# Optimization experiments

Hardware: AMD Instinct MI355X
Metric: run time of the kernel (lower is better)

## Reference

```python
import jax, jax.numpy as jnp
import numpy as np

D_EMBED = 768
D_HEAD = 64
B, S = 4, 4096


def setup_inputs() -> dict:
    key = jax.random.key(0)
    ks = jax.random.split(key, 8)
    x = jax.random.normal(ks[0], (B, S, D_EMBED), dtype=jnp.float32)
    mask = jax.random.randint(ks[1], (B, S), 0, 2, dtype=jnp.int32)
    s = 1.0 / np.sqrt(D_EMBED)
    Wq = jax.random.normal(ks[2], (D_EMBED, D_HEAD), dtype=jnp.float32) * s
    bq = jnp.zeros((D_HEAD,), dtype=jnp.float32)
    Wk = jax.random.normal(ks[3], (D_EMBED, D_HEAD), dtype=jnp.float32) * s
    bk = jnp.zeros((D_HEAD,), dtype=jnp.float32)
    Wv = jax.random.normal(ks[4], (D_EMBED, D_HEAD), dtype=jnp.float32) * s
    bv = jnp.zeros((D_HEAD,), dtype=jnp.float32)
    return {"x": x, "mask": mask, "Wq": Wq, "bq": bq, "Wk": Wk, "bk": bk, "Wv": Wv, "bv": bv}


def reference(x, mask, Wq, bq, Wk, bk, Wv, bv):
    # x: [B,S,D_EMBED], mask: [B,S] (0 = masked)
    q = x @ Wq + bq          # [B,S,Dh]
    k = x @ Wk + bk
    v = x @ Wv + bv
    scale = jnp.float32(1.0 / np.sqrt(D_HEAD))
    scores = jnp.einsum('bsd,btd->bst', q, k) * scale   # [B,S,S]
    scores = jnp.where(mask[:, None, :] == 0, jnp.float32(-1e9), scores)
    probs = jax.nn.softmax(scores, axis=-1)
    return jnp.einsum('bst,btd->bsd', probs, v)          # [B,S,Dh]
```

## Files before the change

### kernel.cpp

```cpp
#include <hip/hip_runtime.h>
#include <hip/hip_bf16.h>
#include <hip/hip_fp16.h>
#include <stdint.h>

#define B_  4
#define S_  4096
#define DE  768
#define DH  64
#define NQKV 192
#define MFIX 8.0f
#define NSPLIT 8
#define QG 128

typedef __attribute__((ext_vector_type(8))) short    short8;
typedef __attribute__((ext_vector_type(4))) float    floatx4;
typedef __attribute__((ext_vector_type(4))) unsigned short ushort4v;

__device__ unsigned short g_wt[NQKV * DE];
__device__ unsigned short g_q [B_ * S_ * DH];
__device__ unsigned short g_k [B_ * S_ * DH];
__device__ unsigned short g_vt[B_ * DH * S_];
__device__ unsigned short g_mb[B_ * S_];
__device__ __half g_po[(size_t)B_ * (S_ / QG) * NSPLIT * QG * DH];
__device__ float  g_pl[(size_t)B_ * (S_ / QG) * NSPLIT * QG];

__device__ __forceinline__ unsigned short f2bf_h(float f) {
    union { float f; uint32_t u; } v; v.f = f;
    return (unsigned short)((v.u + 0x8000u) >> 16);
}

__global__ __launch_bounds__(256) void pack_w(
    const float* __restrict__ Wq, const float* __restrict__ Wk,
    const float* __restrict__ Wv, const int* __restrict__ mask)
{
    int idx = blockIdx.x * 256 + threadIdx.x;
    if (idx < B_ * S_)
        g_mb[idx] = mask[idx] ? (unsigned short)0x3F80 : (unsigned short)0;
    if (idx >= NQKV * DE) return;
    int n = idx / DE;
    int d = idx - n * DE;
    float w;
    if      (n < 64)  w = Wq[d * 64 + n];
    else if (n < 128) w = Wk[d * 64 + (n - 64)];
    else              w = Wv[d * 64 + (n - 128)];
    g_wt[idx] = f2bf_h(w);
}

__global__ __launch_bounds__(256, 3) void qkv_mfma(
    const float* __restrict__ x,
    const float* __restrict__ bq, const float* __restrict__ bk,
    const float* __restrict__ bv)
{
    __shared__ unsigned short xs[32][776];
    const int t    = threadIdx.x;
    const int lane = t & 63;
    const int wave = t >> 6;
    const int c16  = lane & 15;
    const int quad = lane >> 4;
    const int n0   = wave * 48;
    const int row0 = blockIdx.x * 32;

    {
        const int xr = t >> 3;
        const int xc = t & 7;
        const float* xrow = x + (size_t)(row0 + xr) * DE;
        #pragma unroll
        for (int j = 0; j < 24; ++j) {
            int c4 = xc + 8 * j;
            floatx4 v = *(const floatx4*)&xrow[c4 * 4];
            ushort4v h;
            #pragma unroll
            for (int k = 0; k < 4; ++k) h[k] = f2bf_h(v[k]);
            *(ushort4v*)&xs[xr][c4 * 4] = h;
        }
    }
    __syncthreads();

    floatx4 acc[6];
    #pragma unroll
    for (int i = 0; i < 6; ++i) acc[i] = (floatx4){0.f,0.f,0.f,0.f};

    short8 wb[6];
    #pragma unroll
    for (int nt = 0; nt < 3; ++nt) {
        const unsigned short* wrow = g_wt + (size_t)(n0 + nt * 16 + c16) * DE + quad * 8;
        wb[2 * nt]     = *(const short8*)wrow;
        wb[2 * nt + 1] = *(const short8*)(wrow + 32);
    }

    #pragma unroll
    for (int ks = 0; ks < 12; ++ks) {
        const int k0  = ks * 64;
        const int k0n = (ks < 11) ? k0 + 64 : 0;
        short8 nwb[6];
        #pragma unroll
        for (int nt = 0; nt < 3; ++nt) {
            const unsigned short* wrow = g_wt + (size_t)(n0 + nt * 16 + c16) * DE + k0n + quad * 8;
            nwb[2 * nt]     = *(const short8*)wrow;
            nwb[2 * nt + 1] = *(const short8*)(wrow + 32);
        }
        short8 a00 = *(const short8*)&xs[c16][k0 + quad * 8];
        short8 a01 = *(const short8*)&xs[c16][k0 + quad * 8 + 32];
        short8 a10 = *(const short8*)&xs[16 + c16][k0 + quad * 8];
        short8 a11 = *(const short8*)&xs[16 + c16][k0 + quad * 8 + 32];
        #pragma unroll
        for (int nt = 0; nt < 3; ++nt) {
            acc[nt]     = __builtin_amdgcn_mfma_f32_16x16x32_bf16(a00, wb[2 * nt],     acc[nt],     0, 0, 0);
            acc[nt]     = __builtin_amdgcn_mfma_f32_16x16x32_bf16(a01, wb[2 * nt + 1], acc[nt],     0, 0, 0);
            acc[3 + nt] = __builtin_amdgcn_mfma_f32_16x16x32_bf16(a10, wb[2 * nt],     acc[3 + nt], 0, 0, 0);
            acc[3 + nt] = __builtin_amdgcn_mfma_f32_16x16x32_bf16(a11, wb[2 * nt + 1], acc[3 + nt], 0, 0, 0);
        }
        #pragma unroll
        for (int j = 0; j < 6; ++j) wb[j] = nwb[j];
    }

    #pragma unroll
    for (int m = 0; m < 2; ++m) {
        const int tokb = row0 + m * 16 + quad * 4;
        #pragma unroll
        for (int nt = 0; nt < 3; ++nt) {
            int n = n0 + nt * 16 + c16;
            int which = n >> 6;
            int d = n & 63;
            float bias = (which == 0) ? bq[d] : (which == 1) ? bk[d] : bv[d];
            floatx4 a = acc[m * 3 + nt];
            if (which == 0) {
                #pragma unroll
                for (int r = 0; r < 4; ++r)
                    g_q[(size_t)(tokb + r) * DH + d] = f2bf_h((a[r] + bias) * 0.125f);
            } else if (which == 1) {
                #pragma unroll
                for (int r = 0; r < 4; ++r)
                    g_k[(size_t)(tokb + r) * DH + d] = f2bf_h(a[r] + bias);
            } else {
                ushort4v h;
                #pragma unroll
                for (int r = 0; r < 4; ++r) h[r] = f2bf_h(a[r] + bias);
                int b = tokb >> 12;
                int tloc = tokb & (S_ - 1);
                int w = tloc & 63;
                int p = 32 * (w >> 5) + 8 * ((w >> 2) & 3) + 4 * ((w >> 4) & 1);
                *(ushort4v*)&g_vt[((size_t)b * DH + d) * S_ + (tloc & ~63) + p] = h;
            }
        }
    }
}

__global__ __launch_bounds__(256, 4) void attn_kernel()
{
    __shared__ short8 ksv[2][512];
    __shared__ short8 vsv[2][512];

    const int t    = threadIdx.x;
    const int lane = t & 63;
    const int wave = t >> 6;
    const int c16  = lane & 15;
    const int quad = lane >> 4;
    const int qg   = blockIdx.x;
    const int b    = blockIdx.y;
    const int s    = blockIdx.z;
    const size_t tok0 = (size_t)b * S_;
    const int pidx = (b * (S_ / QG) + qg) * NSPLIT + s;

    const unsigned short* kbase = g_k + tok0 * DH;
    const unsigned short* vtb   = g_vt + (size_t)b * DH * S_;
    const unsigned short* mbrow = g_mb + b * S_;

    short8 aq0A, aq1A, aq0B, aq1B;
    {
        const unsigned short* qrA = g_q + (tok0 + qg * QG + wave * 32 + c16) * DH;
        aq0A = *(const short8*)(qrA + quad * 8);
        aq1A = *(const short8*)(qrA + quad * 8 + 32);
        const unsigned short* qrB = qrA + 16 * DH;
        aq0B = *(const short8*)(qrB + quad * 8);
        aq1B = *(const short8*)(qrB + quad * 8 + 32);
    }

    short8 ones;
    #pragma unroll
    for (int j = 0; j < 8; ++j) ones[j] = (short)0x3F80;

    floatx4 acc[2][5];
    #pragma unroll
    for (int qt = 0; qt < 2; ++qt)
        #pragma unroll
        for (int i = 0; i < 5; ++i) acc[qt][i] = (floatx4){0.f,0.f,0.f,0.f};

    const int kbeg = s * (S_ / NSPLIT);
    const int NT   = (S_ / NSPLIT) / 64;

    const int p0 = wave * 128 + lane;
    const int p1 = p0 + 64;
    const int r0 = p0 >> 3, cc0 = (p0 & 7) ^ (r0 & 7);
    const int r1 = p1 >> 3, cc1 = (p1 & 7) ^ (r1 & 7);

    #define STAGE(tbs, buf)                                                              \
    do {                                                                                 \
        const unsigned short* kg0 = kbase + (size_t)((tbs) + r0) * DH + cc0 * 8;         \
        const unsigned short* kg1 = kbase + (size_t)((tbs) + r1) * DH + cc1 * 8;         \
        const unsigned short* vg0 = vtb + (size_t)r0 * S_ + (tbs) + cc0 * 8;             \
        const unsigned short* vg1 = vtb + (size_t)r1 * S_ + (tbs) + cc1 * 8;             \
        __builtin_amdgcn_global_load_lds(                                                \
            (const __attribute__((address_space(1))) uint32_t*)kg0,                      \
            (__attribute__((address_space(3))) uint32_t*)&ksv[buf][wave * 128], 16, 0, 0);\
        __builtin_amdgcn_global_load_lds(                                                \
            (const __attribute__((address_space(1))) uint32_t*)kg1,                      \
            (__attribute__((address_space(3))) uint32_t*)&ksv[buf][wave * 128 + 64], 16, 0, 0);\
        __builtin_amdgcn_global_load_lds(                                                \
            (const __attribute__((address_space(1))) uint32_t*)vg0,                      \
            (__attribute__((address_space(3))) uint32_t*)&vsv[buf][wave * 128], 16, 0, 0);\
        __builtin_amdgcn_global_load_lds(                                                \
            (const __attribute__((address_space(1))) uint32_t*)vg1,                      \
            (__attribute__((address_space(3))) uint32_t*)&vsv[buf][wave * 128 + 64], 16, 0, 0);\
    } while (0)

    STAGE(kbeg, 0);

    for (int i = 0; i < NT; ++i) {
        const int tb = kbeg + i * 64;
        __syncthreads();

        ushort4v mv[4];
        #pragma unroll
        for (int nt = 0; nt < 4; ++nt)
            mv[nt] = *(const ushort4v*)&mbrow[tb + nt * 16 + quad * 4];

        if (i + 1 < NT) STAGE(tb + 64, (i + 1) & 1);

        const short8* kcur = ksv[i & 1];
        const short8* vcur = vsv[i & 1];

        short8 pfA[2], pfB[2];
        #pragma unroll
        for (int nt = 0; nt < 4; ++nt) {
            const int key = c16 + 16 * nt;
            short8 kb0 = kcur[key * 8 + (quad ^ (key & 7))];
            short8 kb1 = kcur[key * 8 + ((quad + 4) ^ (key & 7))];
            floatx4 zA = (floatx4){0.f,0.f,0.f,0.f};
            zA = __builtin_amdgcn_mfma_f32_16x16x32_bf16(kb0, aq0A, zA, 0, 0, 0);
            zA = __builtin_amdgcn_mfma_f32_16x16x32_bf16(kb1, aq1A, zA, 0, 0, 0);
            floatx4 zB = (floatx4){0.f,0.f,0.f,0.f};
            zB = __builtin_amdgcn_mfma_f32_16x16x32_bf16(kb0, aq0B, zB, 0, 0, 0);
            zB = __builtin_amdgcn_mfma_f32_16x16x32_bf16(kb1, aq1B, zB, 0, 0, 0);
            #pragma unroll
            for (int r = 0; r < 4; ++r) {
                union { uint32_t u; float f; } mu;
                mu.u = ((uint32_t)mv[nt][r]) << 16;
                pfA[nt >> 1][(nt & 1) * 4 + r] = (short)f2bf_h(__expf(zA[r] - MFIX) * mu.f);
                pfB[nt >> 1][(nt & 1) * 4 + r] = (short)f2bf_h(__expf(zB[r] - MFIX) * mu.f);
            }
        }

        #pragma unroll
        for (int h = 0; h < 2; ++h) {
            #pragma unroll
            for (int nt = 0; nt < 4; ++nt) {
                const int d = c16 + 16 * nt;
                short8 vb = vcur[d * 8 + ((h * 4 + quad) ^ (d & 7))];
                acc[0][nt] = __builtin_amdgcn_mfma_f32_16x16x32_bf16(vb, pfA[h], acc[0][nt], 0, 0, 0);
                acc[1][nt] = __builtin_amdgcn_mfma_f32_16x16x32_bf16(vb, pfB[h], acc[1][nt], 0, 0, 0);
            }
            acc[0][4] = __builtin_amdgcn_mfma_f32_16x16x32_bf16(ones, pfA[h], acc[0][4], 0, 0, 0);
            acc[1][4] = __builtin_amdgcn_mfma_f32_16x16x32_bf16(ones, pfB[h], acc[1][4], 0, 0, 0);
        }
    }

    unsigned short* po = (unsigned short*)g_po + (size_t)pidx * (QG * DH);
    #pragma unroll
    for (int qt = 0; qt < 2; ++qt) {
        const int qrow = wave * 32 + qt * 16 + c16;
        #pragma unroll
        for (int nt = 0; nt < 4; ++nt) {
            ushort4v hh;
            #pragma unroll
            for (int r = 0; r < 4; ++r)
                hh[r] = __half_as_ushort(__float2half(acc[qt][nt][r]));
            *(ushort4v*)&po[(size_t)qrow * DH + nt * 16 + quad * 4] = hh;
        }
    }
    if (quad == 0) {
        float* pl = g_pl + (size_t)pidx * QG;
        pl[wave * 32 + c16]      = acc[0][4][0];
        pl[wave * 32 + 16 + c16] = acc[1][4][0];
    }
}

__global__ __launch_bounds__(256) void combine(float* __restrict__ out)
{
    const int idx = blockIdx.x * 256 + threadIdx.x;
    const int d4  = idx & 15;
    const int tok = idx >> 4;
    const int qq  = tok & (QG - 1);
    const int qg  = (tok >> 7) & (S_ / QG - 1);
    const int b   = tok >> 12;
    const int base = (b * (S_ / QG) + qg) * NSPLIT;
    floatx4 os = (floatx4){0.f,0.f,0.f,0.f};
    float ls = 0.f;
    #pragma unroll
    for (int s = 0; s < NSPLIT; ++s) {
        const __half* pp = g_po + (size_t)(base + s) * (QG * DH) + qq * 64 + d4 * 4;
        #pragma unroll
        for (int j = 0; j < 4; ++j) os[j] += __half2float(pp[j]);
        ls += g_pl[(size_t)(base + s) * QG + qq];
    }
    float inv = 1.0f / ls;
    floatx4 r;
    #pragma unroll
    for (int j = 0; j < 4; ++j) r[j] = os[j] * inv;
    *(floatx4*)&out[(size_t)tok * DH + d4 * 4] = r;
}

extern "C" void kernel_launch(void* const* d_in, const int* in_sizes, int n_in,
                              void* d_out, int out_size, void* d_ws, size_t ws_size,
                              hipStream_t stream) {
    const float* x   = (const float*)d_in[0];
    const int*   msk = (const int*)  d_in[1];
    const float* Wq  = (const float*)d_in[2];
    const float* bq  = (const float*)d_in[3];
    const float* Wk  = (const float*)d_in[4];
    const float* bk  = (const float*)d_in[5];
    const float* Wv  = (const float*)d_in[6];
    const float* bv  = (const float*)d_in[7];
    float* out = (float*)d_out;

    pack_w<<<dim3((NQKV * DE + 255) / 256), 256, 0, stream>>>(Wq, Wk, Wv, msk);
    qkv_mfma<<<dim3(B_ * S_ / 32), 256, 0, stream>>>(x, bq, bk, bv);
    attn_kernel<<<dim3(S_ / QG, B_, NSPLIT), 256, 0, stream>>>();
    combine<<<dim3(B_ * S_ * DH / 1024), 256, 0, stream>>>(out);
}
```

Measured before the change: 147.7 us.

## Compact unmasked keys via prefix scan and skip masked key tiles

A new scan kernel computes, per batch, each unmasked token's position among the unmasked keys and the total count. The QKV projection then writes K and V only for those tokens, packed at their compacted index. Attention iterates over the compacted count split across the 8 slices instead of all 4096 keys, and masks only the padded tail. This removes the work on masked keys, which is about half under the random mask. It adds a serial per-batch scan launch, scattered K/V stores, and setprio around the PV MFMAs. If every key in a row is masked, the result no longer reduces to a uniform average over all keys as the reference does.

```diff
diff --git a/kernel.cpp b/kernel.cpp
--- a/kernel.cpp
+++ b/kernel.cpp
@@ -20,7 +20,8 @@
 __device__ unsigned short g_q [B_ * S_ * DH];
 __device__ unsigned short g_k [B_ * S_ * DH];
 __device__ unsigned short g_vt[B_ * DH * S_];
-__device__ unsigned short g_mb[B_ * S_];
+__device__ int g_ci [B_ * S_];
+__device__ int g_cnt[B_];
 __device__ __half g_po[(size_t)B_ * (S_ / QG) * NSPLIT * QG * DH];
 __device__ float  g_pl[(size_t)B_ * (S_ / QG) * NSPLIT * QG];
 
@@ -31,11 +32,9 @@
 
 __global__ __launch_bounds__(256) void pack_w(
     const float* __restrict__ Wq, const float* __restrict__ Wk,
-    const float* __restrict__ Wv, const int* __restrict__ mask)
+    const float* __restrict__ Wv)
 {
     int idx = blockIdx.x * 256 + threadIdx.x;
-    if (idx < B_ * S_)
-        g_mb[idx] = mask[idx] ? (unsigned short)0x3F80 : (unsigned short)0;
     if (idx >= NQKV * DE) return;
     int n = idx / DE;
     int d = idx - n * DE;
@@ -46,6 +45,29 @@
     g_wt[idx] = f2bf_h(w);
 }
 
+__global__ __launch_bounds__(64) void scan_mask(const int* __restrict__ mask)
+{
+    const int b    = blockIdx.x;
+    const int lane = threadIdx.x;
+    const int* mrow = mask + b * S_;
+    const int base  = lane * 64;
+    int c = 0;
+    for (int j = 0; j < 64; ++j) c += (mrow[base + j] != 0);
+    int inc = c;
+    #pragma unroll
+    for (int d = 1; d < 64; d <<= 1) {
+        int v = __shfl_up(inc, d, 64);
+        if (lane >= d) inc += v;
+    }
+    int run = inc - c;
+    for (int j = 0; j < 64; ++j) {
+        int m = (mrow[base + j] != 0);
+        g_ci[b * S_ + base + j] = m ? run : -1;
+        run += m;
+    }
+    if (lane == 63) g_cnt[b] = inc;
+}
+
 __global__ __launch_bounds__(256, 3) void qkv_mfma(
     const float* __restrict__ x,
     const float* __restrict__ bq, const float* __restrict__ bk,
@@ -117,6 +139,7 @@
     #pragma unroll
     for (int m = 0; m < 2; ++m) {
         const int tokb = row0 + m * 16 + quad * 4;
+        const int bb   = tokb >> 12;
         #pragma unroll
         for (int nt = 0; nt < 3; ++nt) {
             int n = n0 + nt * 16 + c16;
@@ -130,17 +153,21 @@
                     g_q[(size_t)(tokb + r) * DH + d] = f2bf_h((a[r] + bias) * 0.125f);
             } else if (which == 1) {
                 #pragma unroll
-                for (int r = 0; r < 4; ++r)
-                    g_k[(size_t)(tokb + r) * DH + d] = f2bf_h(a[r] + bias);
+                for (int r = 0; r < 4; ++r) {
+                    int ci = g_ci[tokb + r];
+                    if (ci >= 0)
+                        g_k[((size_t)bb * S_ + ci) * DH + d] = f2bf_h(a[r] + bias);
+                }
             } else {
-                ushort4v h;
                 #pragma unroll
-                for (int r = 0; r < 4; ++r) h[r] = f2bf_h(a[r] + bias);
-                int b = tokb >> 12;
-                int tloc = tokb & (S_ - 1);
-                int w = tloc & 63;
-                int p = 32 * (w >> 5) + 8 * ((w >> 2) & 3) + 4 * ((w >> 4) & 1);
-                *(ushort4v*)&g_vt[((size_t)b * DH + d) * S_ + (tloc & ~63) + p] = h;
+                for (int r = 0; r < 4; ++r) {
+                    int ci = g_ci[tokb + r];
+                    if (ci >= 0) {
+                        int w = ci & 63;
+                        int p = 32 * (w >> 5) + 8 * ((w >> 2) & 3) + 4 * ((w >> 4) & 1) + (w & 3);
+                        g_vt[((size_t)bb * DH + d) * S_ + (ci & ~63) + p] = f2bf_h(a[r] + bias);
+                    }
+                }
             }
         }
     }
@@ -164,7 +191,14 @@
 
     const unsigned short* kbase = g_k + tok0 * DH;
     const unsigned short* vtb   = g_vt + (size_t)b * DH * S_;
-    const unsigned short* mbrow = g_mb + b * S_;
+
+    const int cnt = g_cnt[b];
+    const int c64 = (cnt + 63) & ~63;
+    const int CH  = ((c64 + NSPLIT * 64 - 1) / (NSPLIT * 64)) * 64;
+    const int kbeg = s * CH;
+    int kend = kbeg + CH;
+    if (kend > c64) kend = c64;
+    const int NT = (kend > kbeg) ? (kend - kbeg) >> 6 : 0;
 
     short8 aq0A, aq1A, aq0B, aq1B;
     {
@@ -185,9 +219,6 @@
     for (int qt = 0; qt < 2; ++qt)
         #pragma unroll
         for (int i = 0; i < 5; ++i) acc[qt][i] = (floatx4){0.f,0.f,0.f,0.f};
-
-    const int kbeg = s * (S_ / NSPLIT);
-    const int NT   = (S_ / NSPLIT) / 64;
 
     const int p0 = wave * 128 + lane;
     const int p1 = p0 + 64;
@@ -214,16 +245,11 @@
             (__attribute__((address_space(3))) uint32_t*)&vsv[buf][wave * 128 + 64], 16, 0, 0);\
     } while (0)
 
-    STAGE(kbeg, 0);
+    if (NT > 0) STAGE(kbeg, 0);
 
     for (int i = 0; i < NT; ++i) {
         const int tb = kbeg + i * 64;
         __syncthreads();
-
-        ushort4v mv[4];
-        #pragma unroll
-        for (int nt = 0; nt < 4; ++nt)
-            mv[nt] = *(const ushort4v*)&mbrow[tb + nt * 16 + quad * 4];
 
         if (i + 1 < NT) STAGE(tb + 64, (i + 1) & 1);
 
@@ -244,13 +270,14 @@
             zB = __builtin_amdgcn_mfma_f32_16x16x32_bf16(kb1, aq1B, zB, 0, 0, 0);
             #pragma unroll
             for (int r = 0; r < 4; ++r) {
-                union { uint32_t u; float f; } mu;
-                mu.u = ((uint32_t)mv[nt][r]) << 16;
-                pfA[nt >> 1][(nt & 1) * 4 + r] = (short)f2bf_h(__expf(zA[r] - MFIX) * mu.f);
-                pfB[nt >> 1][(nt & 1) * 4 + r] = (short)f2bf_h(__expf(zB[r] - MFIX) * mu.f);
+                const int kpos = tb + 16 * nt + 4 * quad + r;
+                unsigned short mm = (kpos < cnt) ? (unsigned short)0xFFFFu : (unsigned short)0;
+                pfA[nt >> 1][(nt & 1) * 4 + r] = (short)(f2bf_h(__expf(zA[r] - MFIX)) & mm);
+                pfB[nt >> 1][(nt & 1) * 4 + r] = (short)(f2bf_h(__expf(zB[r] - MFIX)) & mm);
             }
         }
 
+        __builtin_amdgcn_s_setprio(1);
         #pragma unroll
         for (int h = 0; h < 2; ++h) {
             #pragma unroll
@@ -263,6 +290,7 @@
             acc[0][4] = __builtin_amdgcn_mfma_f32_16x16x32_bf16(ones, pfA[h], acc[0][4], 0, 0, 0);
             acc[1][4] = __builtin_amdgcn_mfma_f32_16x16x32_bf16(ones, pfB[h], acc[1][4], 0, 0, 0);
         }
+        __builtin_amdgcn_s_setprio(0);
     }
 
     unsigned short* po = (unsigned short*)g_po + (size_t)pidx * (QG * DH);
@@ -323,7 +351,8 @@
     const float* bv  = (const float*)d_in[7];
     float* out = (float*)d_out;
 
-    pack_w<<<dim3((NQKV * DE + 255) / 256), 256, 0, stream>>>(Wq, Wk, Wv, msk);
+    pack_w<<<dim3((NQKV * DE + 255) / 256), 256, 0, stream>>>(Wq, Wk, Wv);
+    scan_mask<<<dim3(B_), 64, 0, stream>>>(msk);
     qkv_mfma<<<dim3(B_ * S_ / 32), 256, 0, stream>>>(x, bq, bk, bv);
     attn_kernel<<<dim3(S_ / QG, B_, NSPLIT), 256, 0, stream>>>();
     combine<<<dim3(B_ * S_ * DH / 1024), 256, 0, stream>>>(out);
```

Measured after the change: 147.8 us. No clear change (+0.1%).
